# Optimization experiments

Measured on AMD Instinct MI355X. Metric: run time of the kernel, lower is better.

## Reference

```python
import jax, jax.numpy as jnp
import numpy as np

EMBED_DIM = 1024
NUM_HEADS = 16
HEAD_DIM = EMBED_DIM // NUM_HEADS


def setup_inputs() -> dict:
    key = jax.random.key(0)
    ks = jax.random.split(key, 9)
    bs, seq_len = 4, 2048
    s = 1.0 / np.sqrt(EMBED_DIM)
    return {
        "x": jax.random.normal(ks[0], (bs, seq_len, EMBED_DIM), jnp.float32),
        "wq": jax.random.uniform(ks[1], (EMBED_DIM, EMBED_DIM), jnp.float32, -s, s),
        "bq": jax.random.uniform(ks[2], (EMBED_DIM,), jnp.float32, -s, s),
        "wk": jax.random.uniform(ks[3], (EMBED_DIM, EMBED_DIM), jnp.float32, -s, s),
        "bk": jax.random.uniform(ks[4], (EMBED_DIM,), jnp.float32, -s, s),
        "wv": jax.random.uniform(ks[5], (EMBED_DIM, EMBED_DIM), jnp.float32, -s, s),
        "bv": jax.random.uniform(ks[6], (EMBED_DIM,), jnp.float32, -s, s),
        "wo": jax.random.uniform(ks[7], (EMBED_DIM, EMBED_DIM), jnp.float32, -s, s),
        "bo": jax.random.uniform(ks[8], (EMBED_DIM,), jnp.float32, -s, s),
    }


def reference(x, wq, bq, wk, bk, wv, bv, wo, bo):
    bs, seq_len, _ = x.shape
    # projections (torch Linear: y = x @ W.T + b; here w stored as [out,in])
    q = x @ wq.T + bq
    k = x @ wk.T + bk
    v = x @ wv.T + bv
    # split heads -> (bs, heads, seq, head_dim)
    def split(t):
        return t.reshape(bs, seq_len, NUM_HEADS, HEAD_DIM).transpose(0, 2, 1, 3)
    q, k, v = split(q), split(k), split(v)
    scale = 1.0 / jnp.sqrt(jnp.asarray(HEAD_DIM, jnp.float32))
    scores = jnp.einsum("bhqd,bhkd->bhqk", q, k) * scale
    attn = jax.nn.softmax(scores, axis=-1)
    out = jnp.einsum("bhqk,bhkd->bhqd", attn, v)
    out = out.transpose(0, 2, 1, 3).reshape(bs, seq_len, EMBED_DIM)
    return out @ wo.T + bo
```

## Files before the change

kernel.cpp:

```cpp
#include <hip/hip_runtime.h>
#include <stdint.h>

#define SEQ 2048
#define BSZ 4
#define NH 16
#define HD 64
#define EMB 1024
#define NT (SEQ / 64)
#define QSCALE 0.1803368801111f

using bf16x8 = __attribute__((ext_vector_type(8))) __bf16;
using u16x8  = __attribute__((ext_vector_type(8))) unsigned short;
using u32x4  = __attribute__((ext_vector_type(4))) uint32_t;
using f32x4  = __attribute__((ext_vector_type(4))) float;
using f32x16 = __attribute__((ext_vector_type(16))) float;

__device__ __forceinline__ float exp2v(float x) { return __builtin_amdgcn_exp2f(x); }

__device__ __forceinline__ unsigned short f2bf(float f) {
    union { float f; uint32_t u; } v; v.f = f;
    uint32_t r = v.u + 0x7fffu + ((v.u >> 16) & 1u);
    return (unsigned short)(r >> 16);
}

__device__ __forceinline__ uint32_t cvtpk(float lo, float hi) {
    uint32_t r;
    asm("v_cvt_pk_bf16_f32 %0, %1, %2" : "=v"(r) : "v"(lo), "v"(hi));
    return r;
}
__device__ __forceinline__ void plswap(uint32_t& a, uint32_t& b) {
    asm volatile("v_permlane32_swap_b32 %0, %1" : "+v"(a), "+v"(b));
}

__device__ __forceinline__ void gload16(void* lds, const void* g) {
    __builtin_amdgcn_global_load_lds(
        (const __attribute__((address_space(1))) void*)g,
        (__attribute__((address_space(3))) void*)lds, 16, 0, 0);
}

__global__ void cast_kernel(const float* __restrict__ s, unsigned short* __restrict__ d, int n) {
    int i = (blockIdx.x * blockDim.x + threadIdx.x) * 4;
    if (i + 3 >= n) {
        for (int j = 0; j < 4 && i + j < n; ++j) d[i + j] = f2bf(s[i + j]);
        return;
    }
    float4 v = *(const float4*)(s + i);
    ushort4 o;
    o.x = f2bf(v.x); o.y = f2bf(v.y); o.z = f2bf(v.z); o.w = f2bf(v.w);
    *(ushort4*)(d + i) = o;
}

__global__ void cast4_kernel(const float* __restrict__ w0, const float* __restrict__ w1,
                             const float* __restrict__ w2, const float* __restrict__ w3,
                             unsigned short* __restrict__ d0, unsigned short* __restrict__ d1,
                             unsigned short* __restrict__ d2, unsigned short* __restrict__ d3) {
    const float* s; unsigned short* d;
    switch (blockIdx.y) {
        case 0:  s = w0; d = d0; break;
        case 1:  s = w1; d = d1; break;
        case 2:  s = w2; d = d2; break;
        default: s = w3; d = d3; break;
    }
    int i = (blockIdx.x * blockDim.x + threadIdx.x) * 4;
    float4 v = *(const float4*)(s + i);
    ushort4 o;
    o.x = f2bf(v.x); o.y = f2bf(v.y); o.z = f2bf(v.z); o.w = f2bf(v.w);
    *(ushort4*)(d + i) = o;
}

template <int MODE>
__global__ __launch_bounds__(256, 2)
void gemm_bt(const unsigned short* __restrict__ A,
             const unsigned short* __restrict__ Bw,
             const float* __restrict__ b0, const float* __restrict__ b1,
             const float* __restrict__ b2,
             void* __restrict__ C0, void* __restrict__ C1, void* __restrict__ C2,
             int M, int N, int Kd) {
    __shared__ unsigned short As[128][64];
    __shared__ unsigned short Bs[128][64];

    const int t    = threadIdx.x;
    const int lane = t & 63;
    const int wid  = t >> 6;
    const int g    = lane >> 4;
    const int lr   = lane & 15;
    const int wm   = wid >> 1, wn = wid & 1;
    const int m0   = blockIdx.x * 128, n0 = blockIdx.y * 128;
    const int srow = lane >> 3;
    const int scol = (lane & 7) * 8;

    f32x4 acc[4][4];
    const f32x4 zero = {0.f, 0.f, 0.f, 0.f};
#pragma unroll
    for (int i = 0; i < 4; ++i)
#pragma unroll
        for (int j = 0; j < 4; ++j) acc[i][j] = zero;

    for (int kt = 0; kt < Kd; kt += 64) {
#pragma unroll
        for (int p = 0; p < 4; ++p) {
            int rowA = wid * 32 + p * 8;
            gload16(&As[rowA][0], A  + (size_t)(m0 + rowA + srow) * Kd + kt + scol);
            gload16(&Bs[rowA][0], Bw + (size_t)(n0 + rowA + srow) * Kd + kt + scol);
        }
        __syncthreads();
#pragma unroll
        for (int ks = 0; ks < 2; ++ks) {
            bf16x8 af[4], bfr[4];
#pragma unroll
            for (int m = 0; m < 4; ++m)
                af[m] = *(const bf16x8*)&As[wm * 64 + m * 16 + lr][ks * 32 + g * 8];
#pragma unroll
            for (int n = 0; n < 4; ++n)
                bfr[n] = *(const bf16x8*)&Bs[wn * 64 + n * 16 + lr][ks * 32 + g * 8];
#pragma unroll
            for (int m = 0; m < 4; ++m)
#pragma unroll
                for (int n = 0; n < 4; ++n)
                    acc[m][n] = __builtin_amdgcn_mfma_f32_16x16x32_bf16(af[m], bfr[n], acc[m][n], 0, 0, 0);
        }
        __syncthreads();
    }

    int seg = MODE == 2 ? (n0 >> 10) : 0;
    if (MODE == 2 && seg == 2) {
        unsigned short* CwT = (unsigned short*)C2;
        int nl = n0 & 1023;
#pragma unroll
        for (int n = 0; n < 4; ++n) {
            int colL = nl + wn * 64 + n * 16 + lr;
            float bv = b2[colL];
#pragma unroll
            for (int m = 0; m < 4; ++m) {
                int rowg = m0 + wm * 64 + m * 16 + g * 4;
                int bb = rowg >> 11, seq = rowg & 2047;
                ushort4 w;
                w.x = f2bf(acc[m][n][0] + bv);
                w.y = f2bf(acc[m][n][1] + bv);
                w.z = f2bf(acc[m][n][2] + bv);
                w.w = f2bf(acc[m][n][3] + bv);
                *(ushort4*)(CwT + ((size_t)(bb * 1024 + colL)) * SEQ + seq) = w;
            }
        }
        return;
    }

    const float* bias;
    unsigned short* Cw = nullptr;
    float* Cf = nullptr;
    float scl = 1.0f;
    int nl;
    if (MODE == 2) {
        bias = seg == 0 ? b0 : b1;
        Cw = (unsigned short*)(seg == 0 ? C0 : C1);
        scl = seg == 0 ? QSCALE : 1.0f;
        nl = n0 & 1023;
    } else {
        bias = b0; Cf = (float*)C0; nl = n0;
    }
#pragma unroll
    for (int n = 0; n < 4; ++n) {
        int colL = nl + wn * 64 + n * 16 + lr;
        float bv = bias[colL];
#pragma unroll
        for (int m = 0; m < 4; ++m) {
            int rowg = m0 + wm * 64 + m * 16 + g * 4;
#pragma unroll
            for (int r = 0; r < 4; ++r) {
                float val = (acc[m][n][r] + bv) * scl;
                if (MODE == 2)
                    Cw[(size_t)(rowg + r) * EMB + colL] = f2bf(val);
                else
                    Cf[(size_t)(rowg + r) * EMB + colL] = val;
            }
        }
    }
}

__global__ __launch_bounds__(512, 4)
void flash_attn(const unsigned short* __restrict__ Q,
                const unsigned short* __restrict__ K,
                const unsigned short* __restrict__ VT,
                unsigned short* __restrict__ O) {
    __shared__ unsigned char KsB[2][64 * 128];
    __shared__ unsigned char VtB[2][64 * 128];

    const int nwg  = gridDim.x * gridDim.y * gridDim.z;
    const int cpx  = nwg >> 3;
    const int bid0 = (blockIdx.z * gridDim.y + blockIdx.y) * gridDim.x + blockIdx.x;
    const int bid  = (bid0 % 8) * cpx + (bid0 / 8);
    const int bx   = bid & (gridDim.x - 1);
    const int h    = (bid >> 3) & 15;
    const int b    = bid >> 7;

    const int t    = threadIdx.x;
    const int wid  = t >> 6;
    const int lane = t & 63;
    const int l31  = lane & 31;
    const int hi   = lane >> 5;
    const int hi16 = hi << 4;
    const int sw   = (l31 & 7) << 4;
    const int qbase = bx * 256 + wid * 32;
    const size_t rowbase = (size_t)b * SEQ;
    const unsigned short* Kh  = K + rowbase * EMB + h * HD;
    const unsigned short* Vth = VT + (size_t)(b * 1024 + h * HD) * SEQ;

    const int grow = t >> 3;
    const int gc16 = (t & 7) ^ (grow & 7);
    const unsigned short* Ksrc0 = Kh  + (size_t)grow * EMB + gc16 * 8;
    const unsigned short* Vsrc0 = Vth + (size_t)grow * SEQ + gc16 * 8;

    bf16x8 qf[4];
#pragma unroll
    for (int db = 0; db < 4; ++db)
        qf[db] = *(const bf16x8*)(Q + (rowbase + qbase + l31) * EMB + h * HD + db * 16 + hi * 8);

    bf16x8 vones;
#pragma unroll
    for (int j = 0; j < 8; ++j) vones[j] = (__bf16)1.0f;

    f32x16 o0, o1, o2;
#pragma unroll
    for (int r = 0; r < 16; ++r) { o0[r] = 0.f; o1[r] = 0.f; o2[r] = 0.f; }
    float me = -1e30f;

    auto issue_tile = [&](int kt) {
        unsigned char* Ks = KsB[kt & 1] + wid * 1024;
        unsigned char* Vt = VtB[kt & 1] + wid * 1024;
        gload16(Ks, Ksrc0 + (size_t)kt * 64 * EMB);
        gload16(Vt, Vsrc0 + kt * 64);
    };
    issue_tile(0);

    for (int kt = 0; kt < NT; ++kt) {
        unsigned char* Ks = KsB[kt & 1];
        unsigned char* Vt = VtB[kt & 1];

        __syncthreads();

        if (kt + 1 < NT) issue_tile(kt + 1);

        f32x16 s0, s1;
#pragma unroll
        for (int r = 0; r < 16; ++r) { s0[r] = 0.f; s1[r] = 0.f; }
        __builtin_amdgcn_s_setprio(1);
#pragma unroll
        for (int db = 0; db < 4; ++db) {
            bf16x8 kf0 = *(const bf16x8*)(Ks + l31 * 128        + ((db * 32 + hi16) ^ sw));
            bf16x8 kf1 = *(const bf16x8*)(Ks + (l31 + 32) * 128 + ((db * 32 + hi16) ^ sw));
            s0 = __builtin_amdgcn_mfma_f32_32x32x16_bf16(kf0, qf[db], s0, 0, 0, 0);
            s1 = __builtin_amdgcn_mfma_f32_32x32x16_bf16(kf1, qf[db], s1, 0, 0, 0);
        }
        __builtin_amdgcn_s_setprio(0);

        float pm = fmaxf(fmaxf(s0[0], s0[1]), s0[2]);
#pragma unroll
        for (int r = 3; r < 15; r += 2) pm = fmaxf(fmaxf(pm, s0[r]), s0[r + 1]);
        pm = fmaxf(pm, s0[15]);
#pragma unroll
        for (int r = 0; r < 16; r += 2) pm = fmaxf(fmaxf(pm, s1[r]), s1[r + 1]);
        pm = fmaxf(pm, __shfl_xor(pm, 32));

        if (!__all(pm - me <= 8.0f)) {
            float mn = fmaxf(me, pm);
            float al = exp2v(me - mn);
            me = mn;
#pragma unroll
            for (int r = 0; r < 16; ++r) {
                int addr = hi16 + (((r & 3) + 8 * (r >> 2)) << 2);
                float ar = __int_as_float(
                    __builtin_amdgcn_ds_bpermute(addr, __float_as_int(al)));
                o0[r] *= ar; o1[r] *= ar; o2[r] *= ar;
            }
        }

        s0 = s0 - me;
        s1 = s1 - me;
#pragma unroll
        for (int r = 0; r < 16; ++r) s0[r] = exp2v(s0[r]);
#pragma unroll
        for (int r = 0; r < 16; ++r) s1[r] = exp2v(s1[r]);

        bf16x8 pa[4];
#pragma unroll
        for (int kb = 0; kb < 2; ++kb) {
            uint32_t dw[8];
#pragma unroll
            for (int i = 0; i < 8; ++i)
                dw[i] = kb == 0 ? cvtpk(s0[2 * i], s0[2 * i + 1])
                                : cvtpk(s1[2 * i], s1[2 * i + 1]);
            plswap(dw[0], dw[2]); plswap(dw[1], dw[3]);
            plswap(dw[4], dw[6]); plswap(dw[5], dw[7]);
            u32x4 w0 = {dw[0], dw[1], dw[2], dw[3]};
            u32x4 w1 = {dw[4], dw[5], dw[6], dw[7]};
            pa[kb * 2]     = __builtin_bit_cast(bf16x8, w0);
            pa[kb * 2 + 1] = __builtin_bit_cast(bf16x8, w1);
        }

        __builtin_amdgcn_s_setprio(1);
#pragma unroll
        for (int kk = 0; kk < 4; ++kk) {
            bf16x8 vf0 = *(const bf16x8*)(Vt + l31 * 128        + ((kk * 32 + hi16) ^ sw));
            bf16x8 vf1 = *(const bf16x8*)(Vt + (l31 + 32) * 128 + ((kk * 32 + hi16) ^ sw));
            o0 = __builtin_amdgcn_mfma_f32_32x32x16_bf16(pa[kk], vf0, o0, 0, 0, 0);
            o1 = __builtin_amdgcn_mfma_f32_32x32x16_bf16(pa[kk], vf1, o1, 0, 0, 0);
            o2 = __builtin_amdgcn_mfma_f32_32x32x16_bf16(pa[kk], vones, o2, 0, 0, 0);
        }
        __builtin_amdgcn_s_setprio(0);
    }

#pragma unroll
    for (int r = 0; r < 16; ++r) {
        float inv = 1.0f / o2[r];
        int q = qbase + (r & 3) + 8 * (r >> 2) + 4 * hi;
        size_t ro = (rowbase + q) * EMB + h * HD;
        O[ro + l31]      = f2bf(o0[r] * inv);
        O[ro + 32 + l31] = f2bf(o1[r] * inv);
    }
}

extern "C" void kernel_launch(void* const* d_in, const int* in_sizes, int n_in,
                              void* d_out, int out_size, void* d_ws, size_t ws_size,
                              hipStream_t stream) {
    const float* x  = (const float*)d_in[0];
    const float* wq = (const float*)d_in[1];
    const float* bq = (const float*)d_in[2];
    const float* wk = (const float*)d_in[3];
    const float* bk = (const float*)d_in[4];
    const float* wv = (const float*)d_in[5];
    const float* bv = (const float*)d_in[6];
    const float* wo = (const float*)d_in[7];
    const float* bo = (const float*)d_in[8];

    char* ws = (char*)d_ws;
    const size_t M = (size_t)BSZ * SEQ;
    unsigned short* xb    = (unsigned short*)ws;
    unsigned short* wqkvb = (unsigned short*)(ws + (size_t)16 * 1024 * 1024);
    unsigned short* wob   = (unsigned short*)(ws + (size_t)22 * 1024 * 1024);
    unsigned short* Qb    = (unsigned short*)(ws + (size_t)24 * 1024 * 1024);
    unsigned short* Kb    = Qb + M * EMB;
    unsigned short* VTb   = Kb + M * EMB;

    const int nX = (int)(M * EMB);
    cast_kernel<<<nX / 1024, 256, 0, stream>>>(x, xb, nX);
    cast4_kernel<<<dim3(1024, 4), 256, 0, stream>>>(
        wq, wk, wv, wo,
        wqkvb, wqkvb + 1024 * 1024, wqkvb + 2 * 1024 * 1024, wob);

    gemm_bt<2><<<dim3(64, 24), 256, 0, stream>>>(xb, wqkvb, bq, bk, bv,
                                                 Qb, Kb, VTb, (int)M, 3 * EMB, EMB);

    flash_attn<<<dim3(SEQ / 256, NH, BSZ), 512, 0, stream>>>(Qb, Kb, VTb, xb);

    gemm_bt<0><<<dim3(64, 8), 256, 0, stream>>>(xb, wob, bo, nullptr, nullptr,
                                                d_out, nullptr, nullptr, (int)M, EMB, EMB);
}
```

Before: 201.3 us.

## Replace QKV projection GEMM with 256x256 eight-phase pipelined kernel

Adds a dedicated QKV GEMM that uses 256x256 tiles, 512 threads and double-buffered swizzled LDS staging via direct global-to-LDS loads. The K loop is split into four MFMA clusters, each interleaved with the next tile's loads and manual waitcnt/barrier control, and MFMA sections run at raised wave priority. The aim is to hide global memory latency, avoid LDS bank conflicts and get more reuse per tile than the old 128x128 GEMM. The generic gemm_bt loses its QKV epilogue, and the bigger tiles give fewer blocks (384), which could hurt occupancy and load balance.

```diff
diff --git a/kernel.cpp b/kernel.cpp
--- a/kernel.cpp
+++ b/kernel.cpp
@@ -68,13 +68,164 @@
     *(ushort4*)(d + i) = o;
 }
 
+__global__ __launch_bounds__(512, 2)
+void gemm_qkv_8ph(const unsigned short* __restrict__ A,
+                  const unsigned short* __restrict__ Bw,
+                  const float* __restrict__ b0, const float* __restrict__ b1,
+                  const float* __restrict__ b2,
+                  unsigned short* __restrict__ Cq, unsigned short* __restrict__ Ck,
+                  unsigned short* __restrict__ CvT) {
+    __shared__ __align__(16) unsigned char Asb[2][2][16384];
+    __shared__ __align__(16) unsigned char Bsb[2][2][16384];
+
+    const int t    = threadIdx.x;
+    const int wid  = t >> 6;
+    const int lane = t & 63;
+    const int g    = lane >> 4;
+    const int lr   = lane & 15;
+    const int wm   = wid >> 2;
+    const int wn   = wid & 3;
+    const int m0   = blockIdx.x * 256;
+    const int n0   = blockIdx.y * 256;
+
+    const int r0 = t >> 2;
+    const int cc = t & 3;
+
+    auto stageA = [&](int buf, int kt, int kh) {
+#pragma unroll
+        for (int j = 0; j < 2; ++j) {
+            int r  = j * 128 + r0;
+            int cg = cc ^ ((r >> 1) & 3);
+            gload16(&Asb[buf][kh][j * 8192 + wid * 1024],
+                    A + (size_t)(m0 + r) * EMB + kt + kh * 32 + cg * 8);
+        }
+    };
+    auto stageB = [&](int buf, int kt, int kh) {
+#pragma unroll
+        for (int j = 0; j < 2; ++j) {
+            int r  = j * 128 + r0;
+            int cg = cc ^ ((r >> 1) & 3);
+            gload16(&Bsb[buf][kh][j * 8192 + wid * 1024],
+                    Bw + (size_t)(n0 + r) * EMB + kt + kh * 32 + cg * 8);
+        }
+    };
+    auto ldA = [&](int buf, int kh, int row) -> bf16x8 {
+        int byte = row * 64 + ((g ^ ((row >> 1) & 3)) << 4);
+        return *(const bf16x8*)(&Asb[buf][kh][byte]);
+    };
+    auto ldB = [&](int buf, int kh, int row) -> bf16x8 {
+        int byte = row * 64 + ((g ^ ((row >> 1) & 3)) << 4);
+        return *(const bf16x8*)(&Bsb[buf][kh][byte]);
+    };
+
+    stageA(0, 0, 0); stageB(0, 0, 0);
+    stageA(0, 0, 1); stageB(0, 0, 1);
+
+    f32x4 acc[8][4];
+#pragma unroll
+    for (int i = 0; i < 8; ++i)
+#pragma unroll
+        for (int j = 0; j < 4; ++j) acc[i][j] = (f32x4){0.f, 0.f, 0.f, 0.f};
+
+    asm volatile("s_waitcnt vmcnt(4)" ::: "memory");
+    __builtin_amdgcn_s_barrier();
+    __builtin_amdgcn_sched_barrier(0);
+
+#define MFMA_CLUSTER(MH)                                                              \
+    do {                                                                              \
+        __builtin_amdgcn_s_setprio(1);                                                \
+        _Pragma("unroll")                                                             \
+        for (int m = 0; m < 4; ++m) {                                                 \
+            _Pragma("unroll")                                                         \
+            for (int n = 0; n < 4; ++n)                                               \
+                acc[(MH) * 4 + m][n] = __builtin_amdgcn_mfma_f32_16x16x32_bf16(       \
+                    af[m], bfr[n], acc[(MH) * 4 + m][n], 0, 0, 0);                    \
+        }                                                                             \
+        __builtin_amdgcn_s_setprio(0);                                                \
+    } while (0)
+
+    for (int ts = 0; ts < 16; ++ts) {
+        const int buf  = ts & 1;
+        const int nbuf = buf ^ 1;
+        const int ktn  = (ts + 1) * 64;
+        const bool more = ts < 15;
+        bf16x8 af[4], bfr[4];
+
+#pragma unroll
+        for (int n = 0; n < 4; ++n) bfr[n] = ldB(buf, 0, wn * 64 + n * 16 + lr);
+#pragma unroll
+        for (int m = 0; m < 4; ++m) af[m] = ldA(buf, 0, wm * 128 + m * 16 + lr);
+        if (more) stageA(nbuf, ktn, 0);
+        __builtin_amdgcn_s_barrier();
+        __builtin_amdgcn_sched_barrier(0);
+        MFMA_CLUSTER(0);
+
+#pragma unroll
+        for (int m = 0; m < 4; ++m) af[m] = ldA(buf, 0, wm * 128 + 64 + m * 16 + lr);
+        if (more) {
+            stageB(nbuf, ktn, 0);
+            asm volatile("s_waitcnt vmcnt(4)" ::: "memory");
+        } else {
+            asm volatile("s_waitcnt vmcnt(0)" ::: "memory");
+        }
+        __builtin_amdgcn_s_barrier();
+        __builtin_amdgcn_sched_barrier(0);
+        MFMA_CLUSTER(1);
+
+#pragma unroll
+        for (int n = 0; n < 4; ++n) bfr[n] = ldB(buf, 1, wn * 64 + n * 16 + lr);
+#pragma unroll
+        for (int m = 0; m < 4; ++m) af[m] = ldA(buf, 1, wm * 128 + m * 16 + lr);
+        if (more) stageA(nbuf, ktn, 1);
+        __builtin_amdgcn_s_barrier();
+        __builtin_amdgcn_sched_barrier(0);
+        MFMA_CLUSTER(0);
+
+#pragma unroll
+        for (int m = 0; m < 4; ++m) af[m] = ldA(buf, 1, wm * 128 + 64 + m * 16 + lr);
+        if (more) stageB(nbuf, ktn, 1);
+        asm volatile("s_waitcnt vmcnt(4)" ::: "memory");
+        __builtin_amdgcn_s_barrier();
+        __builtin_amdgcn_sched_barrier(0);
+        MFMA_CLUSTER(1);
+    }
+#undef MFMA_CLUSTER
+
+#pragma unroll
+    for (int n = 0; n < 4; ++n) {
+        int colG = n0 + wn * 64 + n * 16 + lr;
+        int seg  = colG >> 10;
+        int colL = colG & 1023;
+        const float* bias = seg == 0 ? b0 : (seg == 1 ? b1 : b2);
+        float bv  = bias[colL];
+        float scl = seg == 0 ? QSCALE : 1.0f;
+#pragma unroll
+        for (int mq = 0; mq < 8; ++mq) {
+            int rowg = m0 + wm * 128 + mq * 16 + g * 4;
+            if (seg == 2) {
+                int bb = rowg >> 11, seq = rowg & 2047;
+                ushort4 w;
+                w.x = f2bf(acc[mq][n][0] + bv);
+                w.y = f2bf(acc[mq][n][1] + bv);
+                w.z = f2bf(acc[mq][n][2] + bv);
+                w.w = f2bf(acc[mq][n][3] + bv);
+                *(ushort4*)(CvT + ((size_t)(bb * 1024 + colL)) * SEQ + seq) = w;
+            } else {
+                unsigned short* Cw = seg == 0 ? Cq : Ck;
+#pragma unroll
+                for (int rr = 0; rr < 4; ++rr)
+                    Cw[(size_t)(rowg + rr) * EMB + colL] = f2bf((acc[mq][n][rr] + bv) * scl);
+            }
+        }
+    }
+}
+
 template <int MODE>
 __global__ __launch_bounds__(256, 2)
 void gemm_bt(const unsigned short* __restrict__ A,
              const unsigned short* __restrict__ Bw,
-             const float* __restrict__ b0, const float* __restrict__ b1,
-             const float* __restrict__ b2,
-             void* __restrict__ C0, void* __restrict__ C1, void* __restrict__ C2,
+             const float* __restrict__ b0,
+             void* __restrict__ C0,
              int M, int N, int Kd) {
     __shared__ unsigned short As[128][64];
     __shared__ unsigned short Bs[128][64];
@@ -122,57 +273,16 @@
         __syncthreads();
     }
 
-    int seg = MODE == 2 ? (n0 >> 10) : 0;
-    if (MODE == 2 && seg == 2) {
-        unsigned short* CwT = (unsigned short*)C2;
-        int nl = n0 & 1023;
-#pragma unroll
-        for (int n = 0; n < 4; ++n) {
-            int colL = nl + wn * 64 + n * 16 + lr;
-            float bv = b2[colL];
-#pragma unroll
-            for (int m = 0; m < 4; ++m) {
-                int rowg = m0 + wm * 64 + m * 16 + g * 4;
-                int bb = rowg >> 11, seq = rowg & 2047;
-                ushort4 w;
-                w.x = f2bf(acc[m][n][0] + bv);
-                w.y = f2bf(acc[m][n][1] + bv);
-                w.z = f2bf(acc[m][n][2] + bv);
-                w.w = f2bf(acc[m][n][3] + bv);
-                *(ushort4*)(CwT + ((size_t)(bb * 1024 + colL)) * SEQ + seq) = w;
-            }
-        }
-        return;
-    }
-
-    const float* bias;
-    unsigned short* Cw = nullptr;
-    float* Cf = nullptr;
-    float scl = 1.0f;
-    int nl;
-    if (MODE == 2) {
-        bias = seg == 0 ? b0 : b1;
-        Cw = (unsigned short*)(seg == 0 ? C0 : C1);
-        scl = seg == 0 ? QSCALE : 1.0f;
-        nl = n0 & 1023;
-    } else {
-        bias = b0; Cf = (float*)C0; nl = n0;
-    }
 #pragma unroll
     for (int n = 0; n < 4; ++n) {
-        int colL = nl + wn * 64 + n * 16 + lr;
-        float bv = bias[colL];
+        int colg = n0 + wn * 64 + n * 16 + lr;
+        float bv = b0[colg];
 #pragma unroll
         for (int m = 0; m < 4; ++m) {
             int rowg = m0 + wm * 64 + m * 16 + g * 4;
 #pragma unroll
-            for (int r = 0; r < 4; ++r) {
-                float val = (acc[m][n][r] + bv) * scl;
-                if (MODE == 2)
-                    Cw[(size_t)(rowg + r) * EMB + colL] = f2bf(val);
-                else
-                    Cf[(size_t)(rowg + r) * EMB + colL] = val;
-            }
+            for (int r = 0; r < 4; ++r)
+                ((float*)C0)[(size_t)(rowg + r) * N + colg] = acc[m][n][r] + bv;
         }
     }
 }
@@ -347,11 +457,11 @@
         wq, wk, wv, wo,
         wqkvb, wqkvb + 1024 * 1024, wqkvb + 2 * 1024 * 1024, wob);
 
-    gemm_bt<2><<<dim3(64, 24), 256, 0, stream>>>(xb, wqkvb, bq, bk, bv,
-                                                 Qb, Kb, VTb, (int)M, 3 * EMB, EMB);
+    gemm_qkv_8ph<<<dim3(32, 12), 512, 0, stream>>>(xb, wqkvb, bq, bk, bv,
+                                                   Qb, Kb, VTb);
 
     flash_attn<<<dim3(SEQ / 256, NH, BSZ), 512, 0, stream>>>(Qb, Kb, VTb, xb);
 
-    gemm_bt<0><<<dim3(64, 8), 256, 0, stream>>>(xb, wob, bo, nullptr, nullptr,
-                                                d_out, nullptr, nullptr, (int)M, EMB, EMB);
-}
+    gemm_bt<0><<<dim3(64, 8), 256, 0, stream>>>(xb, wob, bo,
+                                                d_out, (int)M, EMB, EMB);
+}
```

Result: slower. 216.1 us (+7.4%).
